# Performance work log

Hardware: AMD Instinct MI355X
Metric: run time of the kernel (lower is better)

## Reference

```python
import jax, jax.numpy as jnp
import numpy as np

N, E, G = 100000, 1600000, 500
F_IN, H, OUT, MD = 128, 128, 1, 30


def gcn_conv(x, src, dst, ew, W, b):
    # PyG GCNConv: x' = D^-1/2 (A + I) D^-1/2 (x W) + b, with edge weights ew
    n = x.shape[0]
    h = x @ W  # [N, H]
    loops = jnp.arange(n)
    s = jnp.concatenate([src, loops])
    d = jnp.concatenate([dst, loops])
    w = jnp.concatenate([ew, jnp.ones((n,), dtype=x.dtype)])
    deg = jax.ops.segment_sum(w, d, num_segments=n)
    dinv = jnp.where(deg > 0, jax.lax.rsqrt(deg), 0.0).astype(x.dtype)
    norm = dinv[s] * w * dinv[d]  # [E+N]
    out = jax.ops.segment_sum(norm[:, None] * h[s], d, num_segments=n)
    return out + b


def setup_inputs() -> dict:
    key = jax.random.key(0)
    ks = jax.random.split(key, 12)
    x = jax.random.normal(ks[0], (N, F_IN), dtype=jnp.float32)
    edge_index = jax.random.randint(ks[1], (2, E), 0, N, dtype=jnp.int64)
    edge_attr = jax.random.uniform(ks[2], (E,), dtype=jnp.float32)
    batch = jnp.sort(jax.random.randint(ks[3], (N,), 0, G, dtype=jnp.int64))
    metadata = jax.random.normal(ks[4], (G, MD), dtype=jnp.float32)
    s = lambda fi, fo: 1.0 / np.sqrt(fi)
    W1 = jax.random.normal(ks[5], (F_IN, H), dtype=jnp.float32) * s(F_IN, H)
    b1 = jnp.zeros((H,), dtype=jnp.float32)
    W2 = jax.random.normal(ks[6], (H, H), dtype=jnp.float32) * s(H, H)
    b2 = jnp.zeros((H,), dtype=jnp.float32)
    Wm = jax.random.normal(ks[7], (MD, H), dtype=jnp.float32) * s(MD, H)
    bm = jnp.zeros((H,), dtype=jnp.float32)
    Wf = jax.random.normal(ks[8], (2 * H, OUT), dtype=jnp.float32) * s(2 * H, OUT)
    bf = jnp.zeros((OUT,), dtype=jnp.float32)
    return {"x": x, "edge_index": edge_index, "edge_attr": edge_attr,
            "batch": batch, "metadata": metadata,
            "W1": W1, "b1": b1, "W2": W2, "b2": b2,
            "Wm": Wm, "bm": bm, "Wf": Wf, "bf": bf}


def reference(x, edge_index, edge_attr, batch, metadata, W1, b1, W2, b2, Wm, bm, Wf, bf):
    src, dst = edge_index[0], edge_index[1]
    h = jax.nn.relu(gcn_conv(x, src, dst, edge_attr, W1, b1))
    h = jax.nn.relu(gcn_conv(h, src, dst, edge_attr, W2, b2))
    # global_mean_pool over batch ids
    sums = jax.ops.segment_sum(h, batch, num_segments=G)
    cnt = jax.ops.segment_sum(jnp.ones((h.shape[0],), h.dtype), batch, num_segments=G)
    pooled = sums / jnp.maximum(cnt, 1.0)[:, None]  # [G, H]
    # per-graph metadata: first node index of graph i, idx = first_node % M
    first_node = jax.ops.segment_min(jnp.arange(batch.shape[0]), batch, num_segments=G)
    idx = first_node % metadata.shape[0]
    md = metadata[idx]  # [G, MD]
    md = jax.nn.relu(md @ Wm + bm)  # dropout inactive at eval
    z = jnp.concatenate([pooled, md], axis=1)
    return z @ Wf + bf
```

## Files before the change

kernel.cpp:

```cpp
#include <hip/hip_runtime.h>
#include <cstdint>


#define BK_SHIFT 9
#define BK_NODES 512
#define CH 4096
#define NODE_BITS 17
#define NODE_MASK ((1 << NODE_BITS) - 1)

typedef short bf16x8 __attribute__((ext_vector_type(8)));
typedef float f32x4 __attribute__((ext_vector_type(4)));

union bfpack {
    uint4 u;
    bf16x8 b;
};

static __device__ __forceinline__ unsigned int f2bf(float f) {
    unsigned int u = __float_as_uint(f);
    return (u + 0x7fffu + ((u >> 16) & 1u)) >> 16;
}
static __device__ __forceinline__ unsigned int packbf2(float a, float b) {
    return f2bf(a) | (f2bf(b) << 16);
}
static __device__ __forceinline__ float bf_lo(unsigned int v) {
    return __uint_as_float(v << 16);
}
static __device__ __forceinline__ float bf_hi(unsigned int v) {
    return __uint_as_float(v & 0xffff0000u);
}

__global__ void k_init_small(int* gstart, int* gend, int G, int* bcnt, int NBK) {
    int g = blockIdx.x * blockDim.x + threadIdx.x;
    if (g < G) { gstart[g] = 0x7fffffff; gend[g] = 0; }
    if (g < NBK) bcnt[g] = 0;
}

__global__ void k_init_nodes(const int* __restrict__ batch,
                             int* __restrict__ gstart, int* __restrict__ gend, int N) {
    int i = blockIdx.x * blockDim.x + threadIdx.x;
    if (i >= N) return;
    int b = batch[i];
    if (i == 0 || batch[i - 1] != b) gstart[b] = i;
    if (i == N - 1 || batch[i + 1] != b) gend[b] = i + 1;
}

__global__ __launch_bounds__(256) void k_binhist(const int* __restrict__ dst, int E,
                                                 int* __restrict__ bcnt, int NBK) {
    __shared__ int h[256];
    int tid = threadIdx.x;
    h[tid] = 0;
    __syncthreads();
    int base = blockIdx.x * CH;
    int nend = min(base + CH, E);
    for (int i = base + tid; i < nend; i += 256) atomicAdd(&h[dst[i] >> BK_SHIFT], 1);
    __syncthreads();
    if (tid < NBK && h[tid]) atomicAdd(&bcnt[tid], h[tid]);
}

__global__ __launch_bounds__(256) void k_binscan(const int* __restrict__ bcnt,
                                                 int* __restrict__ bbase,
                                                 int* __restrict__ bfill, int NBK) {
    __shared__ int sc[256];
    int tid = threadIdx.x;
    int v = (tid < NBK) ? bcnt[tid] : 0;
    sc[tid] = v;
    __syncthreads();
    for (int d = 1; d < 256; d <<= 1) {
        int t = (tid >= d) ? sc[tid - d] : 0;
        __syncthreads();
        sc[tid] += t;
        __syncthreads();
    }
    int excl = sc[tid] - v;
    if (tid < NBK) { bbase[tid] = excl; bfill[tid] = excl; }
    if (tid == 255) bbase[NBK] = sc[255];
}

__global__ __launch_bounds__(256) void k_binscatter(const int* __restrict__ src,
                                                    const int* __restrict__ dst,
                                                    const float* __restrict__ ew,
                                                    int* __restrict__ bfill,
                                                    int2* __restrict__ binned, int E) {
    __shared__ int2 stage2[CH];
    __shared__ unsigned char bkt2[CH];
    __shared__ int hist[256], sc[256], lofs[256], cnt2[256], gbase[256];
    int tid = threadIdx.x;
    int base = blockIdx.x * CH;
    int n = min(CH, E - base);
    hist[tid] = 0;
    cnt2[tid] = 0;
    __syncthreads();
    int2 ev[CH / 256];
    int bk[CH / 256];
#pragma unroll
    for (int j = 0; j < CH / 256; ++j) {
        int i = base + tid + j * 256;
        bk[j] = -1;
        if (i < base + n) {
            int s = src[i], d = dst[i];
            float w = ew[i];
            int b = d >> BK_SHIFT;
            ev[j] = make_int2(s | ((d & (BK_NODES - 1)) << NODE_BITS), __float_as_int(w));
            bk[j] = b;
            atomicAdd(&hist[b], 1);
        }
    }
    __syncthreads();
    int hv = hist[tid];
    sc[tid] = hv;
    __syncthreads();
    for (int d = 1; d < 256; d <<= 1) {
        int t = (tid >= d) ? sc[tid - d] : 0;
        __syncthreads();
        sc[tid] += t;
        __syncthreads();
    }
    lofs[tid] = sc[tid] - hv;
    gbase[tid] = hv ? atomicAdd(&bfill[tid], hv) : 0;
    __syncthreads();
#pragma unroll
    for (int j = 0; j < CH / 256; ++j) {
        if (bk[j] >= 0) {
            int r = atomicAdd(&cnt2[bk[j]], 1);
            int p = lofs[bk[j]] + r;
            stage2[p] = ev[j];
            bkt2[p] = (unsigned char)bk[j];
        }
    }
    __syncthreads();
    for (int i = tid; i < n; i += 256) {
        int b = bkt2[i];
        binned[gbase[b] + (i - lofs[b])] = stage2[i];
    }
}

__global__ __launch_bounds__(256) void k_csr(const int2* __restrict__ binned,
                                             const int* __restrict__ bbase,
                                             int2* __restrict__ cvb,
                                             int* __restrict__ rowptr,
                                             float* __restrict__ dinv, int N, int E) {
    __shared__ int lh[BK_NODES];
    __shared__ float ls[BK_NODES];
    __shared__ int lofs[BK_NODES];
    __shared__ int s2[256];
    int tid = threadIdx.x;
    int b = blockIdx.x;
    int nbase = b << BK_SHIFT;
    int nend = min(nbase + BK_NODES, N);
    int ebase = bbase[b], eend = bbase[b + 1];
    for (int i = tid; i < BK_NODES; i += 256) { lh[i] = 0; ls[i] = 0.f; }
    __syncthreads();
    for (int e = ebase + tid; e < eend; e += 256) {
        int2 v = binned[e];
        int local = (v.x >> NODE_BITS) & (BK_NODES - 1);
        atomicAdd(&lh[local], 1);
        atomicAdd(&ls[local], __int_as_float(v.y));
    }
    __syncthreads();
    int p0 = lh[2 * tid], p1 = lh[2 * tid + 1];
    int pv = p0 + p1;
    s2[tid] = pv;
    __syncthreads();
    for (int d = 1; d < 256; d <<= 1) {
        int t = (tid >= d) ? s2[tid - d] : 0;
        __syncthreads();
        s2[tid] += t;
        __syncthreads();
    }
    int e2 = s2[tid] - pv;
    lofs[2 * tid] = e2;
    lofs[2 * tid + 1] = e2 + p0;
    __syncthreads();
    for (int i = nbase + tid; i < nend; i += 256) {
        int local = i - nbase;
        rowptr[i] = ebase + lofs[local];
        dinv[i] = rsqrtf(1.0f + ls[local]);
    }
    if (b == 0 && tid == 0) rowptr[N] = E;
    __syncthreads();
    for (int e = ebase + tid; e < eend; e += 256) {
        int2 v = binned[e];
        int local = (v.x >> NODE_BITS) & (BK_NODES - 1);
        int r = atomicAdd(&lofs[local], 1);
        cvb[ebase + r] = make_int2(v.x & NODE_MASK, v.y);
    }
}

__global__ __launch_bounds__(256) void k_wt(const float* __restrict__ W,
                                            unsigned short* __restrict__ WT) {
    int idx = blockIdx.x * 256 + threadIdx.x;
    int n = idx >> 7, k = idx & 127;
    WT[idx] = (unsigned short)f2bf(W[(size_t)k * 128 + n]);
}

__global__ __launch_bounds__(256) void k_gemm1(const float* __restrict__ X,
                                               const unsigned short* __restrict__ WT,
                                               const float* __restrict__ dinv,
                                               unsigned short* __restrict__ Y, int M) {
    int tid = threadIdx.x;
    int wid = tid >> 6, lane = tid & 63;
    int rowb = blockIdx.x * 64 + wid * 16;
    int r16 = lane & 15, kg = lane >> 4;
    int arow = min(rowb + r16, M - 1);
    const float* xr = X + (size_t)arow * 128 + kg * 8;
    bf16x8 a[4];
#pragma unroll
    for (int kc = 0; kc < 4; ++kc) {
        float4 u = *reinterpret_cast<const float4*>(xr + kc * 32);
        float4 v = *reinterpret_cast<const float4*>(xr + kc * 32 + 4);
        bfpack pk;
        pk.u = make_uint4(packbf2(u.x, u.y), packbf2(u.z, u.w),
                          packbf2(v.x, v.y), packbf2(v.z, v.w));
        a[kc] = pk.b;
    }
    float dv[4];
#pragma unroll
    for (int r = 0; r < 4; ++r) {
        int ro = rowb + kg * 4 + r;
        dv[r] = (ro < M) ? dinv[ro] : 0.f;
    }
    const bf16x8* Bp = reinterpret_cast<const bf16x8*>(WT + (size_t)r16 * 128 + kg * 8);
#pragma unroll
    for (int nt = 0; nt < 8; ++nt) {
        const bf16x8* B = Bp + (size_t)nt * 256;
        f32x4 acc = {0.f, 0.f, 0.f, 0.f};
        acc = __builtin_amdgcn_mfma_f32_16x16x32_bf16(a[0], B[0], acc, 0, 0, 0);
        acc = __builtin_amdgcn_mfma_f32_16x16x32_bf16(a[1], B[4], acc, 0, 0, 0);
        acc = __builtin_amdgcn_mfma_f32_16x16x32_bf16(a[2], B[8], acc, 0, 0, 0);
        acc = __builtin_amdgcn_mfma_f32_16x16x32_bf16(a[3], B[12], acc, 0, 0, 0);
        int colo = nt * 16 + r16;
#pragma unroll
        for (int r = 0; r < 4; ++r) {
            int ro = rowb + kg * 4 + r;
            if (ro < M) Y[(size_t)ro * 128 + colo] = (unsigned short)f2bf(acc[r] * dv[r]);
        }
    }
}

__global__ __launch_bounds__(256) void k_gemm(const unsigned short* __restrict__ Xb,
                                              const unsigned short* __restrict__ WT,
                                              const float* __restrict__ dinv,
                                              unsigned short* __restrict__ Y, int M) {
    int tid = threadIdx.x;
    int wid = tid >> 6, lane = tid & 63;
    int rowb = blockIdx.x * 64 + wid * 16;
    int r16 = lane & 15, kg = lane >> 4;
    const bf16x8* Ap = reinterpret_cast<const bf16x8*>(Xb + (size_t)(rowb + r16) * 128 + kg * 8);
    bf16x8 a0 = Ap[0], a1 = Ap[4], a2 = Ap[8], a3 = Ap[12];
    float dv[4];
#pragma unroll
    for (int r = 0; r < 4; ++r) {
        int ro = rowb + kg * 4 + r;
        dv[r] = (ro < M) ? dinv[ro] : 0.f;
    }
    const bf16x8* Bp = reinterpret_cast<const bf16x8*>(WT + (size_t)r16 * 128 + kg * 8);
#pragma unroll
    for (int nt = 0; nt < 8; ++nt) {
        const bf16x8* B = Bp + (size_t)nt * 256;
        f32x4 acc = {0.f, 0.f, 0.f, 0.f};
        acc = __builtin_amdgcn_mfma_f32_16x16x32_bf16(a0, B[0], acc, 0, 0, 0);
        acc = __builtin_amdgcn_mfma_f32_16x16x32_bf16(a1, B[4], acc, 0, 0, 0);
        acc = __builtin_amdgcn_mfma_f32_16x16x32_bf16(a2, B[8], acc, 0, 0, 0);
        acc = __builtin_amdgcn_mfma_f32_16x16x32_bf16(a3, B[12], acc, 0, 0, 0);
        int colo = nt * 16 + r16;
#pragma unroll
        for (int r = 0; r < 4; ++r) {
            int ro = rowb + kg * 4 + r;
            if (ro < M) Y[(size_t)ro * 128 + colo] = (unsigned short)f2bf(acc[r] * dv[r]);
        }
    }
}

__global__ __launch_bounds__(256) void k_agg(const unsigned int* __restrict__ Hb,
                                             const int* __restrict__ rowptr,
                                             const int2* __restrict__ cvb,
                                             const float* __restrict__ dinv,
                                             const float* __restrict__ bias,
                                             unsigned int* __restrict__ OutB, int N) {
    __shared__ int2 lcv[4][4][64];
    int lane = threadIdx.x & 63;
    int wid = threadIdx.x >> 6;
    int grp = blockIdx.x * 4 + wid;
    int n0 = grp * 4;
    if (n0 >= N) return;
    int r0 = rowptr[n0];
    int r1 = rowptr[min(n0 + 1, N)];
    int r2 = rowptr[min(n0 + 2, N)];
    int r3 = rowptr[min(n0 + 3, N)];
    int r4 = rowptr[min(n0 + 4, N)];
    int c0 = r1 - r0, c1 = r2 - r1, c2 = r3 - r2, c3 = r4 - r3;
    bool v1n = n0 + 1 < N, v2n = n0 + 2 < N, v3n = n0 + 3 < N;
    unsigned int hv0 = Hb[(size_t)n0 * 64 + lane];
    unsigned int hv1 = v1n ? Hb[(size_t)(n0 + 1) * 64 + lane] : 0u;
    unsigned int hv2 = v2n ? Hb[(size_t)(n0 + 2) * 64 + lane] : 0u;
    unsigned int hv3 = v3n ? Hb[(size_t)(n0 + 3) * 64 + lane] : 0u;
    float a00 = bf_lo(hv0), a01 = bf_hi(hv0);
    float a10 = bf_lo(hv1), a11 = bf_hi(hv1);
    float a20 = bf_lo(hv2), a21 = bf_hi(hv2);
    float a30 = bf_lo(hv3), a31 = bf_hi(hv3);
    int nmax = max(max(c0, c1), max(c2, c3));
    for (int base = 0; base < nmax; base += 64) {
        int bl = base + lane;
        int2 t0 = (bl < c0) ? cvb[r0 + bl] : make_int2(0, 0);
        int2 t1 = (bl < c1) ? cvb[r1 + bl] : make_int2(0, 0);
        int2 t2 = (bl < c2) ? cvb[r2 + bl] : make_int2(0, 0);
        int2 t3 = (bl < c3) ? cvb[r3 + bl] : make_int2(0, 0);
        lcv[wid][0][lane] = t0;
        lcv[wid][1][lane] = t1;
        lcv[wid][2][lane] = t2;
        lcv[wid][3][lane] = t3;
        int m = min(64, nmax - base);
        for (int j0 = 0; j0 < m; j0 += 8) {
#pragma unroll
            for (int jj = 0; jj < 8; ++jj) {
                int j = j0 + jj;
                if (j < m) {
                    int2 e0 = lcv[wid][0][j];
                    int2 e1 = lcv[wid][1][j];
                    int2 e2 = lcv[wid][2][j];
                    int2 e3 = lcv[wid][3][j];
                    unsigned int h0 = Hb[(size_t)e0.x * 64 + lane];
                    unsigned int h1 = Hb[(size_t)e1.x * 64 + lane];
                    unsigned int h2 = Hb[(size_t)e2.x * 64 + lane];
                    unsigned int h3 = Hb[(size_t)e3.x * 64 + lane];
                    float w0 = __int_as_float(e0.y);
                    float w1 = __int_as_float(e1.y);
                    float w2 = __int_as_float(e2.y);
                    float w3 = __int_as_float(e3.y);
                    a00 = fmaf(w0, bf_lo(h0), a00);
                    a01 = fmaf(w0, bf_hi(h0), a01);
                    a10 = fmaf(w1, bf_lo(h1), a10);
                    a11 = fmaf(w1, bf_hi(h1), a11);
                    a20 = fmaf(w2, bf_lo(h2), a20);
                    a21 = fmaf(w2, bf_hi(h2), a21);
                    a30 = fmaf(w3, bf_lo(h3), a30);
                    a31 = fmaf(w3, bf_hi(h3), a31);
                }
            }
        }
    }
    float2 bv = reinterpret_cast<const float2*>(bias)[lane];
    float d0 = dinv[n0];
    a00 = fmaxf(fmaf(a00, d0, bv.x), 0.f);
    a01 = fmaxf(fmaf(a01, d0, bv.y), 0.f);
    OutB[(size_t)n0 * 64 + lane] = packbf2(a00, a01);
    if (v1n) {
        float d1 = dinv[n0 + 1];
        a10 = fmaxf(fmaf(a10, d1, bv.x), 0.f);
        a11 = fmaxf(fmaf(a11, d1, bv.y), 0.f);
        OutB[(size_t)(n0 + 1) * 64 + lane] = packbf2(a10, a11);
    }
    if (v2n) {
        float d2 = dinv[n0 + 2];
        a20 = fmaxf(fmaf(a20, d2, bv.x), 0.f);
        a21 = fmaxf(fmaf(a21, d2, bv.y), 0.f);
        OutB[(size_t)(n0 + 2) * 64 + lane] = packbf2(a20, a21);
    }
    if (v3n) {
        float d3 = dinv[n0 + 3];
        a30 = fmaxf(fmaf(a30, d3, bv.x), 0.f);
        a31 = fmaxf(fmaf(a31, d3, bv.y), 0.f);
        OutB[(size_t)(n0 + 3) * 64 + lane] = packbf2(a30, a31);
    }
}

__global__ __launch_bounds__(256) void k_poolhead(const unsigned int* __restrict__ H2u,
                                                  const int* __restrict__ gstart,
                                                  const int* __restrict__ gend,
                                                  const float* __restrict__ meta,
                                                  const float* __restrict__ Wm,
                                                  const float* __restrict__ bm,
                                                  const float* __restrict__ Wf,
                                                  const float* __restrict__ bf,
                                                  float* __restrict__ out, int G) {
    int g = blockIdx.x;
    int tid = threadIdx.x;
    int cu = tid & 63, q = tid >> 6;
    __shared__ float r0[256], r1[256];
    __shared__ float pooled[128];
    __shared__ float red[128];
    int b = gstart[g];
    int e = gend[g];
    int cntg = e - b;
    float s0 = 0.f, s1 = 0.f;
    for (int i = q; i < cntg; i += 4) {
        unsigned int v = H2u[(size_t)(b + i) * 64 + cu];
        s0 += bf_lo(v);
        s1 += bf_hi(v);
    }
    r0[tid] = s0; r1[tid] = s1;
    __syncthreads();
    if (tid < 64) {
        float t0 = r0[cu] + r0[cu + 64] + r0[cu + 128] + r0[cu + 192];
        float t1 = r1[cu] + r1[cu + 64] + r1[cu + 128] + r1[cu + 192];
        float inv = 1.f / fmaxf((float)cntg, 1.f);
        pooled[2 * cu] = t0 * inv;
        pooled[2 * cu + 1] = t1 * inv;
    }
    __syncthreads();
    if (tid < 128) {
        int c = tid;
        int idx = gstart[g] % G;
        float m = bm[c];
#pragma unroll
        for (int k = 0; k < 30; ++k) m = fmaf(meta[idx * 30 + k], Wm[k * 128 + c], m);
        m = fmaxf(m, 0.f);
        red[c] = pooled[c] * Wf[c] + m * Wf[128 + c];
    }
    __syncthreads();
    for (int st = 64; st > 0; st >>= 1) {
        if (tid < st) red[tid] += red[tid + st];
        __syncthreads();
    }
    if (tid == 0) out[g] = red[0] + bf[0];
}

extern "C" void kernel_launch(void* const* d_in, const int* in_sizes, int n_in,
                              void* d_out, int out_size, void* d_ws, size_t ws_size,
                              hipStream_t stream) {
    const float* x     = (const float*)d_in[0];
    const int*   ei    = (const int*)d_in[1];
    const float* ew    = (const float*)d_in[2];
    const int*   batch = (const int*)d_in[3];
    const float* meta  = (const float*)d_in[4];
    const float* W1    = (const float*)d_in[5];
    const float* b1    = (const float*)d_in[6];
    const float* W2    = (const float*)d_in[7];
    const float* b2    = (const float*)d_in[8];
    const float* Wm    = (const float*)d_in[9];
    const float* bm    = (const float*)d_in[10];
    const float* Wf    = (const float*)d_in[11];
    const float* bf    = (const float*)d_in[12];

    int N = in_sizes[0] / 128;
    int E = in_sizes[2];
    int G = in_sizes[4] / 30;
    int Mpad = (N + 63) & ~63;
    int NBK = (N + BK_NODES - 1) >> BK_SHIFT;
    const int* srcp = ei;
    const int* dstp = ei + E;

    char* p = (char*)d_ws;
    auto alloc = [&](size_t bytes) -> void* {
        void* r = p;
        p += (bytes + 255) & ~(size_t)255;
        return r;
    };
    float* dinv   = (float*)alloc((size_t)N * 4);
    int*   rowptr = (int*)alloc((size_t)(N + 1) * 4);
    int2*  binned = (int2*)alloc((size_t)E * 8);
    int2*  cvb    = (int2*)alloc((size_t)E * 8);
    int*   bcnt   = (int*)alloc((size_t)NBK * 4);
    int*   bbase  = (int*)alloc((size_t)(NBK + 1) * 4);
    int*   bfillp = (int*)alloc((size_t)NBK * 4);
    unsigned short* H   = (unsigned short*)alloc((size_t)Mpad * 128 * 2);
    unsigned short* H2  = (unsigned short*)alloc((size_t)Mpad * 128 * 2);
    unsigned short* WT1 = (unsigned short*)alloc(128 * 128 * 2);
    unsigned short* WT2 = (unsigned short*)alloc(128 * 128 * 2);
    int*   gstart = (int*)alloc((size_t)G * 4);
    int*   gend   = (int*)alloc((size_t)G * 4);

    int EB = (E + CH - 1) / CH;
    k_init_small<<<(max(G, NBK) + 255) / 256, 256, 0, stream>>>(gstart, gend, G, bcnt, NBK);
    k_init_nodes<<<(N + 255) / 256, 256, 0, stream>>>(batch, gstart, gend, N);
    k_binhist<<<EB, 256, 0, stream>>>(dstp, E, bcnt, NBK);
    k_binscan<<<1, 256, 0, stream>>>(bcnt, bbase, bfillp, NBK);
    k_binscatter<<<EB, 256, 0, stream>>>(srcp, dstp, ew, bfillp, binned, E);
    k_csr<<<NBK, 256, 0, stream>>>(binned, bbase, cvb, rowptr, dinv, N, E);

    k_wt<<<64, 256, 0, stream>>>(W1, WT1);
    k_wt<<<64, 256, 0, stream>>>(W2, WT2);

    k_gemm1<<<Mpad / 64, 256, 0, stream>>>(x, WT1, dinv, H, N);
    k_agg<<<(N + 15) / 16, 256, 0, stream>>>((const unsigned int*)H, rowptr, cvb, dinv, b1,
                                             (unsigned int*)H2, N);
    k_gemm<<<Mpad / 64, 256, 0, stream>>>(H2, WT2, dinv, H, N);
    k_agg<<<(N + 15) / 16, 256, 0, stream>>>((const unsigned int*)H, rowptr, cvb, dinv, b2,
                                             (unsigned int*)H2, N);

    k_poolhead<<<G, 256, 0, stream>>>((const unsigned int*)H2, gstart, gend,
                                      meta, Wm, bm, Wf, bf, (float*)d_out, G);
}
```

Baseline: 299.9 us.

## Process eight nodes per wavefront using half-wave row split with 8-byte gathers

The aggregation kernel now assigns eight destination nodes to each wavefront. Each 32-lane half handles a different node and loads 8 bytes (four bf16 features) per lane instead of 4. Row pointers are loaded once and broadcast with shuffles, and the grid is halved to match. The aim is more memory-level parallelism and wider gather loads per edge. In exchange, each wave makes more cvb loads per chunk and does more divergent work, since the loop now runs to the maximum degree over eight nodes instead of four.

```diff
diff --git a/kernel.cpp b/kernel.cpp
--- a/kernel.cpp
+++ b/kernel.cpp
@@ -272,96 +272,100 @@
     }
 }
 
-__global__ __launch_bounds__(256) void k_agg(const unsigned int* __restrict__ Hb,
+__global__ __launch_bounds__(256) void k_agg(const uint2* __restrict__ Hb2,
                                              const int* __restrict__ rowptr,
                                              const int2* __restrict__ cvb,
                                              const float* __restrict__ dinv,
                                              const float* __restrict__ bias,
-                                             unsigned int* __restrict__ OutB, int N) {
-    __shared__ int2 lcv[4][4][64];
-    int lane = threadIdx.x & 63;
-    int wid = threadIdx.x >> 6;
-    int grp = blockIdx.x * 4 + wid;
-    int n0 = grp * 4;
+                                             uint2* __restrict__ OutB2, int N) {
+    __shared__ int2 lcv[4][4][2][64];
+    int tid = threadIdx.x;
+    int lane = tid & 63, wid = tid >> 6;
+    int half = lane >> 5, sl = lane & 31;
+    int n0 = (blockIdx.x * 4 + wid) * 8;
     if (n0 >= N) return;
-    int r0 = rowptr[n0];
-    int r1 = rowptr[min(n0 + 1, N)];
-    int r2 = rowptr[min(n0 + 2, N)];
-    int r3 = rowptr[min(n0 + 3, N)];
-    int r4 = rowptr[min(n0 + 4, N)];
-    int c0 = r1 - r0, c1 = r2 - r1, c2 = r3 - r2, c3 = r4 - r3;
-    bool v1n = n0 + 1 < N, v2n = n0 + 2 < N, v3n = n0 + 3 < N;
-    unsigned int hv0 = Hb[(size_t)n0 * 64 + lane];
-    unsigned int hv1 = v1n ? Hb[(size_t)(n0 + 1) * 64 + lane] : 0u;
-    unsigned int hv2 = v2n ? Hb[(size_t)(n0 + 2) * 64 + lane] : 0u;
-    unsigned int hv3 = v3n ? Hb[(size_t)(n0 + 3) * 64 + lane] : 0u;
-    float a00 = bf_lo(hv0), a01 = bf_hi(hv0);
-    float a10 = bf_lo(hv1), a11 = bf_hi(hv1);
-    float a20 = bf_lo(hv2), a21 = bf_hi(hv2);
-    float a30 = bf_lo(hv3), a31 = bf_hi(hv3);
-    int nmax = max(max(c0, c1), max(c2, c3));
+    int rv = rowptr[min(n0 + min(lane, 8), N)];
+    int rp[9];
+#pragma unroll
+    for (int k = 0; k < 9; ++k) rp[k] = __shfl(rv, k);
+    int cnt[8];
+    int nmax = 0;
+#pragma unroll
+    for (int k = 0; k < 8; ++k) {
+        cnt[k] = rp[k + 1] - rp[k];
+        nmax = max(nmax, cnt[k]);
+    }
+    float a[4][4];
+#pragma unroll
+    for (int s = 0; s < 4; ++s) {
+        int ns = n0 + 2 * s + half;
+        uint2 hv = (ns < N) ? Hb2[(size_t)ns * 32 + sl] : make_uint2(0u, 0u);
+        a[s][0] = bf_lo(hv.x);
+        a[s][1] = bf_hi(hv.x);
+        a[s][2] = bf_lo(hv.y);
+        a[s][3] = bf_hi(hv.y);
+    }
     for (int base = 0; base < nmax; base += 64) {
-        int bl = base + lane;
-        int2 t0 = (bl < c0) ? cvb[r0 + bl] : make_int2(0, 0);
-        int2 t1 = (bl < c1) ? cvb[r1 + bl] : make_int2(0, 0);
-        int2 t2 = (bl < c2) ? cvb[r2 + bl] : make_int2(0, 0);
-        int2 t3 = (bl < c3) ? cvb[r3 + bl] : make_int2(0, 0);
-        lcv[wid][0][lane] = t0;
-        lcv[wid][1][lane] = t1;
-        lcv[wid][2][lane] = t2;
-        lcv[wid][3][lane] = t3;
+#pragma unroll
+        for (int s = 0; s < 4; ++s) {
+#pragma unroll
+            for (int h = 0; h < 2; ++h) {
+                int k = 2 * s + h;
+                int2 t = (base + lane < cnt[k]) ? cvb[rp[k] + base + lane]
+                                                : make_int2(0, 0);
+                lcv[wid][s][h][lane] = t;
+            }
+        }
         int m = min(64, nmax - base);
         for (int j0 = 0; j0 < m; j0 += 8) {
 #pragma unroll
             for (int jj = 0; jj < 8; ++jj) {
                 int j = j0 + jj;
                 if (j < m) {
-                    int2 e0 = lcv[wid][0][j];
-                    int2 e1 = lcv[wid][1][j];
-                    int2 e2 = lcv[wid][2][j];
-                    int2 e3 = lcv[wid][3][j];
-                    unsigned int h0 = Hb[(size_t)e0.x * 64 + lane];
-                    unsigned int h1 = Hb[(size_t)e1.x * 64 + lane];
-                    unsigned int h2 = Hb[(size_t)e2.x * 64 + lane];
-                    unsigned int h3 = Hb[(size_t)e3.x * 64 + lane];
+                    int2 e0 = lcv[wid][0][half][j];
+                    int2 e1 = lcv[wid][1][half][j];
+                    int2 e2 = lcv[wid][2][half][j];
+                    int2 e3 = lcv[wid][3][half][j];
+                    uint2 h0 = Hb2[(size_t)e0.x * 32 + sl];
+                    uint2 h1 = Hb2[(size_t)e1.x * 32 + sl];
+                    uint2 h2 = Hb2[(size_t)e2.x * 32 + sl];
+                    uint2 h3 = Hb2[(size_t)e3.x * 32 + sl];
                     float w0 = __int_as_float(e0.y);
                     float w1 = __int_as_float(e1.y);
                     float w2 = __int_as_float(e2.y);
                     float w3 = __int_as_float(e3.y);
-                    a00 = fmaf(w0, bf_lo(h0), a00);
-                    a01 = fmaf(w0, bf_hi(h0), a01);
-                    a10 = fmaf(w1, bf_lo(h1), a10);
-                    a11 = fmaf(w1, bf_hi(h1), a11);
-                    a20 = fmaf(w2, bf_lo(h2), a20);
-                    a21 = fmaf(w2, bf_hi(h2), a21);
-                    a30 = fmaf(w3, bf_lo(h3), a30);
-                    a31 = fmaf(w3, bf_hi(h3), a31);
+                    a[0][0] = fmaf(w0, bf_lo(h0.x), a[0][0]);
+                    a[0][1] = fmaf(w0, bf_hi(h0.x), a[0][1]);
+                    a[0][2] = fmaf(w0, bf_lo(h0.y), a[0][2]);
+                    a[0][3] = fmaf(w0, bf_hi(h0.y), a[0][3]);
+                    a[1][0] = fmaf(w1, bf_lo(h1.x), a[1][0]);
+                    a[1][1] = fmaf(w1, bf_hi(h1.x), a[1][1]);
+                    a[1][2] = fmaf(w1, bf_lo(h1.y), a[1][2]);
+                    a[1][3] = fmaf(w1, bf_hi(h1.y), a[1][3]);
+                    a[2][0] = fmaf(w2, bf_lo(h2.x), a[2][0]);
+                    a[2][1] = fmaf(w2, bf_hi(h2.x), a[2][1]);
+                    a[2][2] = fmaf(w2, bf_lo(h2.y), a[2][2]);
+                    a[2][3] = fmaf(w2, bf_hi(h2.y), a[2][3]);
+                    a[3][0] = fmaf(w3, bf_lo(h3.x), a[3][0]);
+                    a[3][1] = fmaf(w3, bf_hi(h3.x), a[3][1]);
+                    a[3][2] = fmaf(w3, bf_lo(h3.y), a[3][2]);
+                    a[3][3] = fmaf(w3, bf_hi(h3.y), a[3][3]);
                 }
             }
         }
     }
-    float2 bv = reinterpret_cast<const float2*>(bias)[lane];
-    float d0 = dinv[n0];
-    a00 = fmaxf(fmaf(a00, d0, bv.x), 0.f);
-    a01 = fmaxf(fmaf(a01, d0, bv.y), 0.f);
-    OutB[(size_t)n0 * 64 + lane] = packbf2(a00, a01);
-    if (v1n) {
-        float d1 = dinv[n0 + 1];
-        a10 = fmaxf(fmaf(a10, d1, bv.x), 0.f);
-        a11 = fmaxf(fmaf(a11, d1, bv.y), 0.f);
-        OutB[(size_t)(n0 + 1) * 64 + lane] = packbf2(a10, a11);
-    }
-    if (v2n) {
-        float d2 = dinv[n0 + 2];
-        a20 = fmaxf(fmaf(a20, d2, bv.x), 0.f);
-        a21 = fmaxf(fmaf(a21, d2, bv.y), 0.f);
-        OutB[(size_t)(n0 + 2) * 64 + lane] = packbf2(a20, a21);
-    }
-    if (v3n) {
-        float d3 = dinv[n0 + 3];
-        a30 = fmaxf(fmaf(a30, d3, bv.x), 0.f);
-        a31 = fmaxf(fmaf(a31, d3, bv.y), 0.f);
-        OutB[(size_t)(n0 + 3) * 64 + lane] = packbf2(a30, a31);
+    float4 bv = reinterpret_cast<const float4*>(bias)[sl];
+#pragma unroll
+    for (int s = 0; s < 4; ++s) {
+        int ns = n0 + 2 * s + half;
+        if (ns < N) {
+            float d = dinv[ns];
+            float o0 = fmaxf(fmaf(a[s][0], d, bv.x), 0.f);
+            float o1 = fmaxf(fmaf(a[s][1], d, bv.y), 0.f);
+            float o2 = fmaxf(fmaf(a[s][2], d, bv.z), 0.f);
+            float o3 = fmaxf(fmaf(a[s][3], d, bv.w), 0.f);
+            OutB2[(size_t)ns * 32 + sl] = make_uint2(packbf2(o0, o1), packbf2(o2, o3));
+        }
     }
 }
 
@@ -473,11 +477,11 @@
     k_wt<<<64, 256, 0, stream>>>(W2, WT2);
 
     k_gemm1<<<Mpad / 64, 256, 0, stream>>>(x, WT1, dinv, H, N);
-    k_agg<<<(N + 15) / 16, 256, 0, stream>>>((const unsigned int*)H, rowptr, cvb, dinv, b1,
-                                             (unsigned int*)H2, N);
+    k_agg<<<(N + 31) / 32, 256, 0, stream>>>((const uint2*)H, rowptr, cvb, dinv, b1,
+                                             (uint2*)H2, N);
     k_gemm<<<Mpad / 64, 256, 0, stream>>>(H2, WT2, dinv, H, N);
-    k_agg<<<(N + 15) / 16, 256, 0, stream>>>((const unsigned int*)H, rowptr, cvb, dinv, b2,
-                                             (unsigned int*)H2, N);
+    k_agg<<<(N + 31) / 32, 256, 0, stream>>>((const uint2*)H, rowptr, cvb, dinv, b2,
+                                             (uint2*)H2, N);
 
     k_poolhead<<<G, 256, 0, stream>>>((const unsigned int*)H2, gstart, gend,
                                       meta, Wm, bm, Wf, bf, (float*)d_out, G);
```

Measured after the change: 299.1 us. No clear change (-0.3%).
